# Kernel tuning notes

Measured on AMD Instinct MI355X. Metric: run time of the kernel, lower is better.

## Reference

```python
import jax, jax.numpy as jnp
import numpy as np

# ---- model constants (match init_kwargs) ----
NX, NY, H, K, GRID = 32, 1, 64, 3, 5
MID = 2 * H + 1            # 129, middle width of each KAN block
NB = GRID + K              # 8 B-spline basis functions per edge
BATCH = 65536


def _grid_pts():
    # uniform extended grid on [-1, 1] with K extra knots each side: GRID+2K+1 pts
    step = 2.0 / GRID
    return jnp.arange(-K, GRID + K + 1, dtype=jnp.float32) * step - 1.0


def bspline_basis(x):
    """Cox-de Boor B-spline bases. x: [B, I] -> [B, I, GRID+K]."""
    g = _grid_pts()[None, None, :]          # [1,1,P]
    xe = x[..., None]                       # [B,I,1]
    B0 = ((xe >= g[..., :-1]) & (xe < g[..., 1:])).astype(x.dtype)
    Bp = B0
    for p in range(1, K + 1):
        left = (xe - g[..., :-(p + 1)]) / (g[..., p:-1] - g[..., :-(p + 1)])
        right = (g[..., p + 1:] - xe) / (g[..., p + 1:] - g[..., 1:-p])
        Bp = left * Bp[..., :-1] + right * Bp[..., 1:]
    return Bp  # [B, I, NB]


def kan_layer(x, coef, sb, ss, bias):
    """pykan KANLayer: y_o = sum_i sb[i,o]*silu(x_i) + ss[i,o]*spline_io(x_i) + bias_o.
    x: [B,I]; coef: [I,O,NB]; sb, ss: [I,O]; bias: [O]."""
    bs = bspline_basis(x)                                   # [B,I,NB]
    spline = jnp.einsum('bip,iop->bo', bs, coef * ss[:, :, None])
    return jax.nn.silu(x) @ sb + spline + bias


def setup_inputs() -> dict:
    key = jax.random.key(0)
    ks = iter(jax.random.split(key, 40))

    def xavier(k, shape, fan_in, fan_out):
        gain = np.sqrt(2.0)  # relu gain, as in the torch module
        std = gain * np.sqrt(2.0 / (fan_in + fan_out))
        return (std * jax.random.normal(k, shape, dtype=jnp.float32))

    inp = {
        'x': jax.random.normal(next(ks), (BATCH, NX), dtype=jnp.float32),
        'W_in': xavier(next(ks), (NX, H), NX, H),
        'b_in': jnp.zeros((H,), jnp.float32),
        'W_out': xavier(next(ks), (H, NY), H, NY),
    }
    for l in range(2):  # num_hidden_layers KAN blocks, each = 2 KANLayers
        for tag, (din, dout) in [('a', (H, MID)), ('b', (MID, H))]:
            inp[f'coef{l}{tag}'] = xavier(next(ks), (din, dout, NB), din * NB, dout)
            inp[f'sb{l}{tag}'] = xavier(next(ks), (din, dout), din, dout)
            inp[f'ss{l}{tag}'] = jnp.ones((din, dout), jnp.float32)
            inp[f'bias{l}{tag}'] = jnp.zeros((dout,), jnp.float32)
    return inp


def reference(x, W_in, b_in, W_out,
              coef0a, sb0a, ss0a, bias0a, coef0b, sb0b, ss0b, bias0b,
              coef1a, sb1a, ss1a, bias1a, coef1b, sb1b, ss1b, bias1b):
    h = jax.nn.relu(x @ W_in + b_in)
    for (ca, sa, ta, ba, cb, sbb, tb, bb) in (
        (coef0a, sb0a, ss0a, bias0a, coef0b, sb0b, ss0b, bias0b),
        (coef1a, sb1a, ss1a, bias1a, coef1b, sb1b, ss1b, bias1b),
    ):
        h = kan_layer(h, ca, sa, ta, ba)   # H -> 2H+1
        h = kan_layer(h, cb, sbb, tb, bb)  # 2H+1 -> H
    return jax.nn.sigmoid(h @ W_out)       # [B, NY]
```

## Files before the change

kernel.cpp:

```cpp
#include <hip/hip_runtime.h>
#include <math.h>
#include <stdint.h>

#define BATCH 65536
#define TB 128

typedef __fp16   fp16x2  __attribute__((ext_vector_type(2)));
typedef _Float16 half8   __attribute__((ext_vector_type(8)));
typedef float    floatx16 __attribute__((ext_vector_type(16)));

#define SH 68
#define SM 130
#define HM_SLICE (32*SM + 64)

#define WIN 2048
#define KSA 36
#define KSB 76
#define WA (KSA*5*512)
#define WB (KSB*2*512)
#define WTOT (WIN + 2*(WA+WB))

__global__ void setup_weights(
    const float* __restrict__ W_in,
    const float* __restrict__ c0a, const float* __restrict__ sb0a, const float* __restrict__ ss0a,
    const float* __restrict__ c0b, const float* __restrict__ sb0b, const float* __restrict__ ss0b,
    const float* __restrict__ c1a, const float* __restrict__ sb1a, const float* __restrict__ ss1a,
    const float* __restrict__ c1b, const float* __restrict__ sb1b, const float* __restrict__ ss1b,
    _Float16* __restrict__ wt) {
  int idx = blockIdx.x * 256 + threadIdx.x;
  if (idx >= WTOT) return;
  float v = 0.0f;
  if (idx < WIN) {
    int ks = idx >> 10; int nt = (idx >> 9) & 1;
    int q = idx & 511;  int l = q >> 3;   int j = q & 7;
    int n = nt*32 + (l & 31);
    int k = ks*16 + (l >> 5)*8 + j;
    v = W_in[k*64 + n];
  } else {
    int e2   = idx - WIN;
    int pair = (e2 >= WA + WB) ? 1 : 0;
    int e    = e2 - pair * (WA + WB);
    if (e < WA) {
      const float* coef = pair ? c1a : c0a;
      const float* sb   = pair ? sb1a : sb0a;
      const float* ss   = pair ? ss1a : ss0a;
      int ks = e / 2560; int r = e - ks*2560;
      int nt = r >> 9;   int q = r & 511;
      int l  = q >> 3;   int j = q & 7;
      int n  = nt*32 + (l & 31);
      int k  = ks*16 + (l >> 5)*8 + j;
      if (n < 129) {
        if (k < 512) { int i = k >> 3, p = k & 7; v = ss[i*129+n] * coef[(i*129+n)*8 + p]; }
        else         { int i = k - 512; if (i < 64) v = sb[i*129+n]; }
      }
    } else {
      const float* coef = pair ? c1b : c0b;
      const float* sb   = pair ? sb1b : sb0b;
      const float* ss   = pair ? ss1b : ss0b;
      int eb = e - WA;
      int ks = eb >> 10; int r = eb & 1023;
      int nt = r >> 9;   int q = r & 511;
      int l  = q >> 3;   int j = q & 7;
      int n  = nt*32 + (l & 31);
      int k  = ks*16 + (l >> 5)*8 + j;
      if (k < 1032)      { int i = k >> 3, p = k & 7; v = ss[i*64+n] * coef[(i*64+n)*8 + p]; }
      else if (k >= 1040){ int s = k - 1040; if (s < 129) v = sb[s*64+n]; }
    }
  }
  wt[idx] = (_Float16)v;
}

__device__ __forceinline__ half8 feat8(float x) {
  float s  = fmaf(x, 2.5f, 5.5f);
  float mf = floorf(s);
  int   m  = (int)mf;
  float u  = s - mf;
  float t  = 1.0f - u;
  float u2 = u*u;
  float w0 = t*t*t * (1.0f/6.0f);
  float w3 = u2*u * (1.0f/6.0f);
  float w1 = fmaf(u2, fmaf(0.5f, u, -1.0f), 2.0f/3.0f);
  float w2 = 1.0f - w0 - w1 - w3;
  union { fp16x2 h2[2]; uint64_t u64; } P;
  P.h2[0] = __builtin_amdgcn_cvt_pkrtz(w0, w1);
  P.h2[1] = __builtin_amdgcn_cvt_pkrtz(w2, w3);
  uint64_t w01 = ((unsigned)m <= 10u) ? P.u64 : 0ull;
  int sh = (m - 3) * 16;
  uint64_t q0 = (sh >= 0) ? ((sh < 64) ? (w01 << sh) : 0ull) : (w01 >> (-sh));
  uint64_t q1 = (sh >= 64) ? (w01 << (sh - 64))
                           : ((sh > 0) ? (w01 >> (64 - sh)) : 0ull);
  union { uint64_t q[2]; half8 h; } R;
  R.q[0] = q0; R.q[1] = q1;
  return R.h;
}

template<int KSPL, int KSIL, int NT, int SIN, int O, int SOUT>
__device__ __forceinline__ void kan_layer(
    const _Float16* __restrict__ hinw, _Float16* __restrict__ houtw,
    const _Float16* __restrict__ wt, const float* __restrict__ bias, int lane) {
  constexpr int KTOT = KSPL + KSIL;
  static_assert(KTOT % 4 == 0, "KTOT must be a multiple of 4");
  const int ln = lane & 31;
  const int kh = lane >> 5;
  const half8* __restrict__ bp = (const half8*)wt + lane;
  floatx16 acc[NT];
  #pragma unroll
  for (int j = 0; j < NT; ++j)
    #pragma unroll
    for (int e = 0; e < 16; ++e) acc[j][e] = 0.0f;

  half8 B[4][NT];
  #pragma unroll
  for (int d = 0; d < 4; ++d)
    #pragma unroll
    for (int j = 0; j < NT; ++j) B[d][j] = bp[(d*NT + j)*64];

  #pragma unroll 4
  for (int ks = 0; ks < KTOT; ++ks) {
    const int slot = ks & 3;
    half8 A;
    if (ks < KSPL) {
      float xv = (float)hinw[ln*SIN + 2*ks + kh];
      A = feat8(xv);
    } else {
      int sk = ks - KSPL;
      half8 h8 = *(const half8*)&hinw[ln*SIN + sk*16 + kh*8];
      union { fp16x2 h2[4]; half8 v; } Au;
      #pragma unroll
      for (int e = 0; e < 4; ++e) {
        float x0 = (float)h8[2*e], x1 = (float)h8[2*e + 1];
        float s0 = x0 / (1.0f + __expf(-x0));
        float s1 = x1 / (1.0f + __expf(-x1));
        Au.h2[e] = __builtin_amdgcn_cvt_pkrtz(s0, s1);
      }
      A = Au.v;
    }
    half8 Bc[NT];
    #pragma unroll
    for (int j = 0; j < NT; ++j) Bc[j] = B[slot][j];
    const int nks = (ks + 4 < KTOT) ? (ks + 4) : (KTOT - 1);
    #pragma unroll
    for (int j = 0; j < NT; ++j) B[slot][j] = bp[(nks*NT + j)*64];
    #pragma unroll
    for (int j = 0; j < NT; ++j)
      acc[j] = __builtin_amdgcn_mfma_f32_32x32x16_f16(A, Bc[j], acc[j], 0, 0, 0);
  }

  #pragma unroll
  for (int j = 0; j < NT; ++j) {
    int col = j*32 + ln;
    if (col < O) {
      float bv = bias[col];
      #pragma unroll
      for (int r = 0; r < 16; ++r) {
        int row = (r & 3) + 8*(r >> 2) + 4*kh;
        houtw[row*SOUT + col] = (_Float16)(acc[j][r] + bv);
      }
    }
  }
}

extern "C" __global__ void __launch_bounds__(256, 2)
kan_forward(const float* __restrict__ x, const float* __restrict__ b_in,
            const float* __restrict__ W_out, const _Float16* __restrict__ wt,
            const float* __restrict__ bias0a, const float* __restrict__ bias0b,
            const float* __restrict__ bias1a, const float* __restrict__ bias1b,
            float* __restrict__ out) {
  __shared__ _Float16 hM[4][HM_SLICE];
  __shared__ _Float16 hH[4][32*SH];
  const int t    = threadIdx.x;
  const int wv   = t >> 6;
  const int lane = t & 63;
  const int ln   = lane & 31;
  const int kh   = lane >> 5;
  _Float16* hMw = hM[wv];
  _Float16* hHw = hH[wv];
  const int rbase = blockIdx.x * TB + wv * 32;

  hMw[32*SM + lane] = (_Float16)0.0f;
  if (lane < 32) hMw[lane*SM + 129] = (_Float16)0.0f;

  {
    const float* xr = &x[(rbase + ln)*32 + kh*8];
    float4 v0 = *(const float4*)&xr[0];
    float4 v1 = *(const float4*)&xr[4];
    float4 v2 = *(const float4*)&xr[16];
    float4 v3 = *(const float4*)&xr[20];
    union { fp16x2 h2[4]; half8 h8; } A0, A1;
    A0.h2[0] = __builtin_amdgcn_cvt_pkrtz(v0.x, v0.y);
    A0.h2[1] = __builtin_amdgcn_cvt_pkrtz(v0.z, v0.w);
    A0.h2[2] = __builtin_amdgcn_cvt_pkrtz(v1.x, v1.y);
    A0.h2[3] = __builtin_amdgcn_cvt_pkrtz(v1.z, v1.w);
    A1.h2[0] = __builtin_amdgcn_cvt_pkrtz(v2.x, v2.y);
    A1.h2[1] = __builtin_amdgcn_cvt_pkrtz(v2.z, v2.w);
    A1.h2[2] = __builtin_amdgcn_cvt_pkrtz(v3.x, v3.y);
    A1.h2[3] = __builtin_amdgcn_cvt_pkrtz(v3.z, v3.w);
    const half8* bp = (const half8*)wt + lane;
    #pragma unroll
    for (int nt = 0; nt < 2; ++nt) {
      floatx16 a;
      #pragma unroll
      for (int e = 0; e < 16; ++e) a[e] = 0.0f;
      a = __builtin_amdgcn_mfma_f32_32x32x16_f16(A0.h8, bp[nt*64],       a, 0, 0, 0);
      a = __builtin_amdgcn_mfma_f32_32x32x16_f16(A1.h8, bp[(2 + nt)*64], a, 0, 0, 0);
      int col = nt*32 + ln;
      float bv = b_in[col];
      #pragma unroll
      for (int r = 0; r < 16; ++r) {
        int row = (r & 3) + 8*(r >> 2) + 4*kh;
        hHw[row*SH + col] = (_Float16)fmaxf(a[r] + bv, 0.0f);
      }
    }
  }

  kan_layer<32, 4,5,SH,129,SM>(hHw, hMw, wt + WIN,             bias0a, lane);
  kan_layer<65,11,2,SM, 64,SH>(hMw, hHw, wt + WIN + WA,        bias0b, lane);
  kan_layer<32, 4,5,SH,129,SM>(hHw, hMw, wt + WIN + WA + WB,   bias1a, lane);
  kan_layer<65,11,2,SM, 64,SH>(hMw, hHw, wt + WIN + 2*WA + WB, bias1b, lane);

  {
    float s = 0.0f;
    #pragma unroll
    for (int j = 0; j < 32; ++j)
      s = fmaf((float)hHw[ln*SH + kh*32 + j], W_out[kh*32 + j], s);
    s += __shfl_down(s, 32);
    if (lane < 32) out[rbase + ln] = 1.0f / (1.0f + __expf(-s));
  }
}

extern "C" void kernel_launch(void* const* d_in, const int* in_sizes, int n_in,
                              void* d_out, int out_size, void* d_ws, size_t ws_size,
                              hipStream_t stream) {
  const float* x     = (const float*)d_in[0];
  const float* W_in  = (const float*)d_in[1];
  const float* b_in  = (const float*)d_in[2];
  const float* W_out = (const float*)d_in[3];
  const float* c0a = (const float*)d_in[4];  const float* sb0a = (const float*)d_in[5];
  const float* ss0a= (const float*)d_in[6];  const float* bias0a=(const float*)d_in[7];
  const float* c0b = (const float*)d_in[8];  const float* sb0b = (const float*)d_in[9];
  const float* ss0b= (const float*)d_in[10]; const float* bias0b=(const float*)d_in[11];
  const float* c1a = (const float*)d_in[12]; const float* sb1a = (const float*)d_in[13];
  const float* ss1a= (const float*)d_in[14]; const float* bias1a=(const float*)d_in[15];
  const float* c1b = (const float*)d_in[16]; const float* sb1b = (const float*)d_in[17];
  const float* ss1b= (const float*)d_in[18]; const float* bias1b=(const float*)d_in[19];
  float*    out = (float*)d_out;
  _Float16* wt  = (_Float16*)d_ws;

  setup_weights<<<(WTOT + 255)/256, 256, 0, stream>>>(
      W_in, c0a, sb0a, ss0a, c0b, sb0b, ss0b,
      c1a, sb1a, ss1a, c1b, sb1b, ss1b, wt);

  kan_forward<<<BATCH/TB, 256, 0, stream>>>(
      x, b_in, W_out, wt, bias0a, bias0b, bias1a, bias1b, out);
}
```

Baseline: 172.6 us.

## Restructure KAN layer loop: vectorized input loads, split spline/silu loops, 2-deep weight prefetch

The single mixed loop over spline and silu k-steps becomes separate loops. The spline part processes groups of 8 k-steps from two 16-byte LDS loads and picks each half value by shifting. This replaces a scalar fp16 LDS load per k-step and removes the per-iteration branch between spline and silu feature paths. The weight prefetch ring shrinks from 4 to 2 slots to cut register pressure, which leaves less latency hiding for global weight loads.

Result: faster. 165.7 us (-4.0%).

```diff
diff --git a/kernel.cpp b/kernel.cpp
--- a/kernel.cpp
+++ b/kernel.cpp
@@ -94,14 +94,23 @@
   return R.h;
 }
 
+__device__ __forceinline__ float extract_half(uint32_t w, int khs) {
+  union { uint32_t u; _Float16 h[2]; } cv;
+  cv.u = w >> khs;
+  return (float)cv.h[0];
+}
+
 template<int KSPL, int KSIL, int NT, int SIN, int O, int SOUT>
 __device__ __forceinline__ void kan_layer(
     const _Float16* __restrict__ hinw, _Float16* __restrict__ houtw,
     const _Float16* __restrict__ wt, const float* __restrict__ bias, int lane) {
   constexpr int KTOT = KSPL + KSIL;
-  static_assert(KTOT % 4 == 0, "KTOT must be a multiple of 4");
-  const int ln = lane & 31;
-  const int kh = lane >> 5;
+  constexpr int NG   = KSPL / 8;
+  constexpr int KR   = KSPL - NG*8;
+  static_assert(KR == 0 || KR == 1, "remainder must be 0/1");
+  const int ln  = lane & 31;
+  const int kh  = lane >> 5;
+  const int khs = kh << 4;
   const half8* __restrict__ bp = (const half8*)wt + lane;
   floatx16 acc[NT];
   #pragma unroll
@@ -109,41 +118,64 @@
     #pragma unroll
     for (int e = 0; e < 16; ++e) acc[j][e] = 0.0f;
 
-  half8 B[4][NT];
-  #pragma unroll
-  for (int d = 0; d < 4; ++d)
+  half8 B[2][NT];
+  #pragma unroll
+  for (int d = 0; d < 2; ++d)
     #pragma unroll
     for (int j = 0; j < NT; ++j) B[d][j] = bp[(d*NT + j)*64];
 
-  #pragma unroll 4
-  for (int ks = 0; ks < KTOT; ++ks) {
-    const int slot = ks & 3;
-    half8 A;
-    if (ks < KSPL) {
-      float xv = (float)hinw[ln*SIN + 2*ks + kh];
-      A = feat8(xv);
-    } else {
-      int sk = ks - KSPL;
-      half8 h8 = *(const half8*)&hinw[ln*SIN + sk*16 + kh*8];
-      union { fp16x2 h2[4]; half8 v; } Au;
-      #pragma unroll
-      for (int e = 0; e < 4; ++e) {
-        float x0 = (float)h8[2*e], x1 = (float)h8[2*e + 1];
-        float s0 = x0 / (1.0f + __expf(-x0));
-        float s1 = x1 / (1.0f + __expf(-x1));
-        Au.h2[e] = __builtin_amdgcn_cvt_pkrtz(s0, s1);
-      }
-      A = Au.v;
-    }
-    half8 Bc[NT];
-    #pragma unroll
-    for (int j = 0; j < NT; ++j) Bc[j] = B[slot][j];
-    const int nks = (ks + 4 < KTOT) ? (ks + 4) : (KTOT - 1);
-    #pragma unroll
-    for (int j = 0; j < NT; ++j) B[slot][j] = bp[(nks*NT + j)*64];
-    #pragma unroll
-    for (int j = 0; j < NT; ++j)
-      acc[j] = __builtin_amdgcn_mfma_f32_32x32x16_f16(A, Bc[j], acc[j], 0, 0, 0);
+  union H8 { half8 h; uint32_t d[4]; };
+
+  #pragma unroll 1
+  for (int g = 0; g < NG; ++g) {
+    H8 ha, hb;
+    ha.h = *(const half8*)&hinw[ln*SIN + g*16];
+    hb.h = *(const half8*)&hinw[ln*SIN + g*16 + 8];
+    #pragma unroll
+    for (int u = 0; u < 8; ++u) {
+      uint32_t w = (u < 4) ? ha.d[u] : hb.d[u & 3];
+      half8 A = feat8(extract_half(w, khs));
+      #pragma unroll
+      for (int j = 0; j < NT; ++j)
+        acc[j] = __builtin_amdgcn_mfma_f32_32x32x16_f16(A, B[u & 1][j], acc[j], 0, 0, 0);
+      #pragma unroll
+      for (int j = 0; j < NT; ++j)
+        B[u & 1][j] = bp[((g*8 + u + 2)*NT + j)*64];
+    }
+  }
+
+  if (KR == 1) {
+    constexpr int ks = NG*8;
+    H8 hc;
+    hc.h = *(const half8*)&hinw[ln*SIN + ks*2];
+    half8 A = feat8(extract_half(hc.d[0], khs));
+    #pragma unroll
+    for (int j = 0; j < NT; ++j)
+      acc[j] = __builtin_amdgcn_mfma_f32_32x32x16_f16(A, B[ks & 1][j], acc[j], 0, 0, 0);
+    #pragma unroll
+    for (int j = 0; j < NT; ++j)
+      B[ks & 1][j] = bp[((ks + 2)*NT + j)*64];
+  }
+
+  #pragma unroll
+  for (int sk = 0; sk < KSIL; ++sk) {
+    const int ks = KSPL + sk;
+    half8 h8 = *(const half8*)&hinw[ln*SIN + sk*16 + kh*8];
+    union { fp16x2 h2[4]; half8 v; } Au;
+    #pragma unroll
+    for (int e = 0; e < 4; ++e) {
+      float x0 = (float)h8[2*e], x1 = (float)h8[2*e + 1];
+      float s0 = x0 / (1.0f + __expf(-x0));
+      float s1 = x1 / (1.0f + __expf(-x1));
+      Au.h2[e] = __builtin_amdgcn_cvt_pkrtz(s0, s1);
+    }
+    #pragma unroll
+    for (int j = 0; j < NT; ++j)
+      acc[j] = __builtin_amdgcn_mfma_f32_32x32x16_f16(Au.v, B[ks & 1][j], acc[j], 0, 0, 0);
+    const int nks = (ks + 2 < KTOT) ? (ks + 2) : (KTOT - 1);
+    #pragma unroll
+    for (int j = 0; j < NT; ++j)
+      B[ks & 1][j] = bp[(nks*NT + j)*64];
   }
 
   #pragma unroll
```
